# Optimization experiments

Hardware: AMD Instinct MI355X
Metric: run time of the kernel (lower is better)

## Reference

```python
import jax, jax.numpy as jnp
import numpy as np
from jax import lax

C = 16
FIRE_RATE = 0.5
STEP_SIZE = 1.0


def _fixed_kernel():
    _i = np.array([0, 1, 0], dtype=np.float32)
    I = np.outer(_i, _i)
    dx = (np.outer([1, 2, 1], [-1, 0, 1]) / 8.0).astype(np.float32)
    dy = dx.T
    lap = np.array([[0.25, 0.5, 0.25], [0.5, -3, 0.5], [0.25, 0.5, 0.25]], dtype=np.float32)
    av = np.ones((3, 3), dtype=np.float32) / 9.0
    k = np.stack([I, dx, dy, lap, av], -1)            # [3,3,5]
    k = np.tile(k, (1, 1, C))                          # [3,3,5*C], channel-major blocks of 5
    return jnp.asarray(k[:, :, None, :])               # HWIO [3,3,1,5*C]

KERNEL = _fixed_kernel()


def setup_inputs() -> dict:
    key = jax.random.key(0)
    ks = jax.random.split(key, 5)
    B, S = 4, 512
    x = jax.random.normal(ks[0], (B, S, S, C), jnp.float32)
    noise = jax.random.normal(ks[1], (B, S, S, 1), jnp.float32)
    W1 = jax.random.normal(ks[2], (5 * C, 4 * C), jnp.float32) * (1.0 / np.sqrt(5 * C))
    b1 = jnp.zeros((4 * C,), jnp.float32)
    W2 = jax.random.normal(ks[3], (4 * C, 2 * C), jnp.float32) * (1.0 / np.sqrt(4 * C))
    b2 = jnp.zeros((2 * C,), jnp.float32)
    W3 = jax.random.normal(ks[4], (2 * C, C), jnp.float32) * (1.0 / np.sqrt(2 * C))
    b3 = jnp.zeros((C,), jnp.float32)
    return {"x": x, "noise": noise, "W1": W1, "b1": b1, "W2": W2, "b2": b2, "W3": W3, "b3": b3}


def _swish(z):
    return z * jax.nn.sigmoid(z)


def reference(x, noise, W1, b1, W2, b2, W3, b3):
    # perceive: depthwise 3x3 conv with 5 fixed kernels per channel -> [B,H,W,5*C]
    y = lax.conv_general_dilated(
        x, KERNEL, window_strides=(1, 1), padding="SAME",
        dimension_numbers=("NHWC", "HWIO", "NHWC"), feature_group_count=C)
    # 3-layer 1x1 conv MLP
    h = _swish(jnp.einsum("bhwc,cd->bhwd", y, W1) + b1)
    h = _swish(jnp.einsum("bhwc,cd->bhwd", h, W2) + b2)
    dx = (jnp.einsum("bhwc,cd->bhwd", h, W3) + b3) * STEP_SIZE
    # stochastic update mask: normal noise <= fire_rate
    update_mask = (noise <= FIRE_RATE).astype(jnp.float32)  # [B,H,W,1]
    return x + dx * update_mask
```

## Files before the change

kernel.cpp:

```cpp
#include <hip/hip_runtime.h>

typedef __bf16 bf16x8 __attribute__((ext_vector_type(8)));
typedef float f32x16 __attribute__((ext_vector_type(16)));
typedef short short8 __attribute__((ext_vector_type(8)));

#define S 512
#define CH 16

#define ELT(v, c) ((c)==0 ? (v).x : (c)==1 ? (v).y : (c)==2 ? (v).z : (v).w)

__device__ __forceinline__ float swishf(float z) {
    return z * __builtin_amdgcn_rcpf(1.0f + __expf(-z));
}

__global__ void prep_weights(const float* __restrict__ W1, const float* __restrict__ b1,
                             const float* __restrict__ W2, const float* __restrict__ b2,
                             const float* __restrict__ W3, const float* __restrict__ b3,
                             short* __restrict__ wsf, float* __restrict__ wsb)
{
    int idx = blockIdx.x * 256 + threadIdx.x;
    if (idx < 12288) {
        int fi = idx >> 9, rem = idx & 511;
        int lane = rem >> 3, j = rem & 7;
        int col = lane & 31, hi = lane >> 5;
        int jp = (j & 3) + 8 * (j >> 2);
        float v;
        if (fi < 18) {
            int n = fi / 9, s = fi - n * 9;
            int dr = s / 3, dc = s - dr * 3;
            int c = hi * 8 + j;
            const float wgt0 = (dr == 1) ? 2.f : 1.f;
            const float wgt1 = (dc == 1) ? 2.f : 1.f;
            const float dlt0 = (float)(dr - 1);
            const float dlt1 = (float)(dc - 1);
            const float lapm[9] = {0.25f, 0.5f, 0.25f, 0.5f, -3.f, 0.5f, 0.25f, 0.5f, 0.25f};
            float kI  = (s == 4) ? 1.f : 0.f;
            float kdx = wgt0 * dlt1 * 0.125f;
            float kdy = dlt0 * wgt1 * 0.125f;
            float klp = lapm[s];
            float kav = 1.f / 9.f;
            const float* wr = W1 + (c * 5) * 64 + n * 32 + col;
            v = kI * wr[0] + kdx * wr[64] + kdy * wr[128] + klp * wr[192] + kav * wr[256];
        } else if (fi < 22) {
            int t = fi - 18;
            int rowW = (t >> 1) * 32 + 4 * hi + (t & 1) * 16 + jp;
            v = W2[rowW * 32 + col];
        } else {
            int t = fi - 22;
            int rowW = 4 * hi + t * 16 + jp;
            int ch = (col & 3) | (((col >> 3) & 1) << 2) | (((col >> 2) & 1) << 3);
            v = (col < 16) ? W3[rowW * 16 + ch] : 0.0f;
        }
        __bf16 b = (__bf16)v;
        wsf[idx] = __builtin_bit_cast(short, b);
    }
    if (blockIdx.x == 0) {
        int t = threadIdx.x;
        if (t < 64) wsb[t] = b1[t];
        else if (t < 96) wsb[t] = b2[t - 64];
        else if (t < 112) wsb[t] = b3[t - 96];
    }
}

__device__ __forceinline__ void loadrow(const float* __restrict__ xb, int gr, int px0,
                                        int col, int hi, bool edgeStrip, float4 L[3][2])
{
    const bool rv = (unsigned)gr < (unsigned)S;
    const int grc = rv ? gr : (gr < 0 ? 0 : S - 1);
    if (!edgeStrip) {
        const float* rp = xb + ((size_t)grc * S + (px0 + col - 1)) * CH + hi * 8;
#pragma unroll
        for (int dc = 0; dc < 3; ++dc) {
            L[dc][0] = *reinterpret_cast<const float4*>(rp + dc * CH);
            L[dc][1] = *reinterpret_cast<const float4*>(rp + dc * CH + 4);
        }
    } else {
#pragma unroll
        for (int dc = 0; dc < 3; ++dc) {
            int c = px0 + col - 1 + dc;
            bool ok = (unsigned)c < (unsigned)S;
            int cl = min(max(c, 0), S - 1);
            const float* p = xb + ((size_t)grc * S + cl) * CH + hi * 8;
            float4 v0 = *reinterpret_cast<const float4*>(p);
            float4 v1 = *reinterpret_cast<const float4*>(p + 4);
            if (!ok) { v0 = make_float4(0.f, 0.f, 0.f, 0.f); v1 = v0; }
            L[dc][0] = v0; L[dc][1] = v1;
        }
    }
    if (!rv) {
#pragma unroll
        for (int dc = 0; dc < 3; ++dc) {
            L[dc][0] = make_float4(0.f, 0.f, 0.f, 0.f);
            L[dc][1] = L[dc][0];
        }
    }
}

__device__ __forceinline__ short8 cvt2(float4 a, float4 b) {
    short8 f;
    f[0] = __builtin_bit_cast(short, (__bf16)a.x);
    f[1] = __builtin_bit_cast(short, (__bf16)a.y);
    f[2] = __builtin_bit_cast(short, (__bf16)a.z);
    f[3] = __builtin_bit_cast(short, (__bf16)a.w);
    f[4] = __builtin_bit_cast(short, (__bf16)b.x);
    f[5] = __builtin_bit_cast(short, (__bf16)b.y);
    f[6] = __builtin_bit_cast(short, (__bf16)b.z);
    f[7] = __builtin_bit_cast(short, (__bf16)b.w);
    return f;
}

#define NR 8

__global__ __launch_bounds__(256, 3) void nca_fused(
    const float* __restrict__ x, const float* __restrict__ noise,
    const short* __restrict__ wsf, const float* __restrict__ wsb,
    float* __restrict__ out)
{
    __shared__ short wlds[12288];
    {
        const int4* src = reinterpret_cast<const int4*>(wsf);
        int4* dst = reinterpret_cast<int4*>(wlds);
        for (int i = threadIdx.x; i < 1536; i += 256) dst[i] = src[i];
    }
    __syncthreads();

    const int tid = threadIdx.x, bid = blockIdx.x;
    const int wv = tid >> 6, lane = tid & 63;
    const int col = lane & 31, hi = lane >> 5;
    const int st = bid & 15;
    const int rgp = (bid >> 4) & 15;
    const int bb = bid >> 8;
    const int px0 = st * 32;
    const int r0 = (rgp * 4 + wv) * NR;
    const bool edgeStrip = (px0 == 0) || (px0 == 480);
    const float* xb = x + (size_t)bb * S * S * CH;
    const short8* wf = reinterpret_cast<const short8*>(wlds);

    float4 bA = *reinterpret_cast<const float4*>(wsb + 96 + 8 * hi);
    float4 bB = *reinterpret_cast<const float4*>(wsb + 96 + 8 * hi + 4);

    short8 fr[3][3];
    {
        float4 P[3][2];
        loadrow(xb, r0 - 1, px0, col, hi, edgeStrip, P);
#pragma unroll
        for (int dc = 0; dc < 3; ++dc) fr[0][dc] = cvt2(P[dc][0], P[dc][1]);
        loadrow(xb, r0, px0, col, hi, edgeStrip, P);
#pragma unroll
        for (int dc = 0; dc < 3; ++dc) fr[1][dc] = cvt2(P[dc][0], P[dc][1]);
        loadrow(xb, r0 + 1, px0, col, hi, edgeStrip, P);
#pragma unroll
        for (int dc = 0; dc < 3; ++dc) fr[2][dc] = cvt2(P[dc][0], P[dc][1]);
    }

#pragma unroll
    for (int i = 0; i < NR; ++i) {
        const int r = r0 + i;

        float4 NL[3][2];
        loadrow(xb, r + 2, px0, col, hi, edgeStrip, NL);

        const float* cp = xb + ((size_t)r * S + px0 + col) * CH + 8 * hi;
        float4 c0 = *reinterpret_cast<const float4*>(cp);
        float4 c1 = *reinterpret_cast<const float4*>(cp + 4);
        float nz = noise[((size_t)(bb * S + r)) * S + px0 + col];

        f32x16 acc1[2] = {{}, {}};
#pragma unroll
        for (int dr = 0; dr < 3; ++dr)
#pragma unroll
            for (int dc = 0; dc < 3; ++dc) {
                const int s = dr * 3 + dc;
                bf16x8 bfrag = __builtin_bit_cast(bf16x8, fr[(i + dr) % 3][dc]);
                bf16x8 a0 = __builtin_bit_cast(bf16x8, wf[s * 64 + lane]);
                bf16x8 a1 = __builtin_bit_cast(bf16x8, wf[(9 + s) * 64 + lane]);
                acc1[0] = __builtin_amdgcn_mfma_f32_32x32x16_bf16(a0, bfrag, acc1[0], 0, 0, 0);
                acc1[1] = __builtin_amdgcn_mfma_f32_32x32x16_bf16(a1, bfrag, acc1[1], 0, 0, 0);
            }

        short8 b2f[4];
#pragma unroll
        for (int t = 0; t < 4; ++t) {
            int n = t >> 1;
            float4 bq0 = *reinterpret_cast<const float4*>(wsb + n * 32 + 4 * hi + 16 * (t & 1));
            float4 bq1 = *reinterpret_cast<const float4*>(wsb + n * 32 + 4 * hi + 16 * (t & 1) + 8);
#pragma unroll
            for (int j = 0; j < 8; ++j) {
                float bias = (j < 4) ? ELT(bq0, j & 3) : ELT(bq1, j & 3);
                float h = swishf(acc1[n][(t & 1) * 8 + j] + bias);
                b2f[t][j] = __builtin_bit_cast(short, (__bf16)h);
            }
        }

        f32x16 acc2 = {};
#pragma unroll
        for (int t = 0; t < 4; ++t) {
            bf16x8 a = __builtin_bit_cast(bf16x8, wf[(18 + t) * 64 + lane]);
            acc2 = __builtin_amdgcn_mfma_f32_32x32x16_bf16(a, __builtin_bit_cast(bf16x8, b2f[t]), acc2, 0, 0, 0);
        }

        short8 b3f[2];
#pragma unroll
        for (int t = 0; t < 2; ++t) {
            float4 cq0 = *reinterpret_cast<const float4*>(wsb + 64 + 4 * hi + 16 * t);
            float4 cq1 = *reinterpret_cast<const float4*>(wsb + 64 + 4 * hi + 16 * t + 8);
#pragma unroll
            for (int j = 0; j < 8; ++j) {
                float bias = (j < 4) ? ELT(cq0, j & 3) : ELT(cq1, j & 3);
                float h = swishf(acc2[t * 8 + j] + bias);
                b3f[t][j] = __builtin_bit_cast(short, (__bf16)h);
            }
        }

        f32x16 acc3 = {};
#pragma unroll
        for (int t = 0; t < 2; ++t) {
            bf16x8 a = __builtin_bit_cast(bf16x8, wf[(22 + t) * 64 + lane]);
            acc3 = __builtin_amdgcn_mfma_f32_32x32x16_bf16(a, __builtin_bit_cast(bf16x8, b3f[t]), acc3, 0, 0, 0);
        }

        {
            size_t pix = ((size_t)(bb * S + r)) * S + px0 + col;
            float msk = (nz <= 0.5f) ? 1.f : 0.f;
            float4 o0, o1;
            o0.x = c0.x + (acc3[0] + bA.x) * msk;
            o0.y = c0.y + (acc3[1] + bA.y) * msk;
            o0.z = c0.z + (acc3[2] + bA.z) * msk;
            o0.w = c0.w + (acc3[3] + bA.w) * msk;
            o1.x = c1.x + (acc3[4] + bB.x) * msk;
            o1.y = c1.y + (acc3[5] + bB.y) * msk;
            o1.z = c1.z + (acc3[6] + bB.z) * msk;
            o1.w = c1.w + (acc3[7] + bB.w) * msk;
            float* op = out + pix * CH + 8 * hi;
            *reinterpret_cast<float4*>(op) = o0;
            *reinterpret_cast<float4*>(op + 4) = o1;
        }

#pragma unroll
        for (int dc = 0; dc < 3; ++dc)
            fr[i % 3][dc] = cvt2(NL[dc][0], NL[dc][1]);
    }
}

extern "C" void kernel_launch(void* const* d_in, const int* in_sizes, int n_in,
                              void* d_out, int out_size, void* d_ws, size_t ws_size,
                              hipStream_t stream)
{
    const float* x     = (const float*)d_in[0];
    const float* noise = (const float*)d_in[1];
    const float* W1    = (const float*)d_in[2];
    const float* b1    = (const float*)d_in[3];
    const float* W2    = (const float*)d_in[4];
    const float* b2    = (const float*)d_in[5];
    const float* W3    = (const float*)d_in[6];
    const float* b3    = (const float*)d_in[7];
    short* wsf = (short*)d_ws;
    float* wsb = (float*)((char*)d_ws + 24576);
    float* out = (float*)d_out;

    hipLaunchKernelGGL(prep_weights, dim3(48), dim3(256), 0, stream,
                       W1, b1, W2, b2, W3, b3, wsf, wsb);
    hipLaunchKernelGGL(nca_fused, dim3(4 * 16 * 16), dim3(256), 0, stream,
                       x, noise, wsf, wsb, out);
}
```

Before: 208.0 us.

## Halve rows per wave, double grid, XCD-aware block mapping, nontemporal stores

Cuts rows per wave from 8 to 4 and doubles the grid to 2048 blocks, raising the occupancy hint to 4 blocks per CU. Block indices are remapped so the 8 blocks dispatched round-robin across XCDs get adjacent row groups, aiming for better L2 reuse of halo rows. It also skips the dead prefetch of the last row and switches output writes to nontemporal stores to reduce cache pollution. The trade-off is a higher halo reload ratio (6 loaded rows per 4 computed instead of 10 per 8) and tighter register limits.

```diff
diff --git a/kernel.cpp b/kernel.cpp
--- a/kernel.cpp
+++ b/kernel.cpp
@@ -1,6 +1,7 @@
 #include <hip/hip_runtime.h>
 
 typedef __bf16 bf16x8 __attribute__((ext_vector_type(8)));
+typedef float f32x4 __attribute__((ext_vector_type(4)));
 typedef float f32x16 __attribute__((ext_vector_type(16)));
 typedef short short8 __attribute__((ext_vector_type(8)));
 
@@ -109,9 +110,9 @@
     return f;
 }
 
-#define NR 8
-
-__global__ __launch_bounds__(256, 3) void nca_fused(
+#define NR 4
+
+__global__ __launch_bounds__(256, 4) void nca_fused(
     const float* __restrict__ x, const float* __restrict__ noise,
     const short* __restrict__ wsf, const float* __restrict__ wsb,
     float* __restrict__ out)
@@ -127,11 +128,15 @@
     const int tid = threadIdx.x, bid = blockIdx.x;
     const int wv = tid >> 6, lane = tid & 63;
     const int col = lane & 31, hi = lane >> 5;
-    const int st = bid & 15;
-    const int rgp = (bid >> 4) & 15;
-    const int bb = bid >> 8;
+
+    const int xcd = bid & 7;
+    const int k = bid >> 3;
+    const int rg = xcd * 4 + (k & 3);
+    const int sb = k >> 2;
+    const int st = sb & 15;
+    const int bb = sb >> 4;
     const int px0 = st * 32;
-    const int r0 = (rgp * 4 + wv) * NR;
+    const int r0 = rg * 16 + wv * NR;
     const bool edgeStrip = (px0 == 0) || (px0 == 480);
     const float* xb = x + (size_t)bb * S * S * CH;
     const short8* wf = reinterpret_cast<const short8*>(wlds);
@@ -158,7 +163,7 @@
         const int r = r0 + i;
 
         float4 NL[3][2];
-        loadrow(xb, r + 2, px0, col, hi, edgeStrip, NL);
+        if (i + 1 < NR) loadrow(xb, r + 2, px0, col, hi, edgeStrip, NL);
 
         const float* cp = xb + ((size_t)r * S + px0 + col) * CH + 8 * hi;
         float4 c0 = *reinterpret_cast<const float4*>(cp);
@@ -222,23 +227,25 @@
         {
             size_t pix = ((size_t)(bb * S + r)) * S + px0 + col;
             float msk = (nz <= 0.5f) ? 1.f : 0.f;
-            float4 o0, o1;
-            o0.x = c0.x + (acc3[0] + bA.x) * msk;
-            o0.y = c0.y + (acc3[1] + bA.y) * msk;
-            o0.z = c0.z + (acc3[2] + bA.z) * msk;
-            o0.w = c0.w + (acc3[3] + bA.w) * msk;
-            o1.x = c1.x + (acc3[4] + bB.x) * msk;
-            o1.y = c1.y + (acc3[5] + bB.y) * msk;
-            o1.z = c1.z + (acc3[6] + bB.z) * msk;
-            o1.w = c1.w + (acc3[7] + bB.w) * msk;
+            f32x4 o0, o1;
+            o0[0] = c0.x + (acc3[0] + bA.x) * msk;
+            o0[1] = c0.y + (acc3[1] + bA.y) * msk;
+            o0[2] = c0.z + (acc3[2] + bA.z) * msk;
+            o0[3] = c0.w + (acc3[3] + bA.w) * msk;
+            o1[0] = c1.x + (acc3[4] + bB.x) * msk;
+            o1[1] = c1.y + (acc3[5] + bB.y) * msk;
+            o1[2] = c1.z + (acc3[6] + bB.z) * msk;
+            o1[3] = c1.w + (acc3[7] + bB.w) * msk;
             float* op = out + pix * CH + 8 * hi;
-            *reinterpret_cast<float4*>(op) = o0;
-            *reinterpret_cast<float4*>(op + 4) = o1;
-        }
-
-#pragma unroll
-        for (int dc = 0; dc < 3; ++dc)
-            fr[i % 3][dc] = cvt2(NL[dc][0], NL[dc][1]);
+            __builtin_nontemporal_store(o0, reinterpret_cast<f32x4*>(op));
+            __builtin_nontemporal_store(o1, reinterpret_cast<f32x4*>(op + 4));
+        }
+
+        if (i + 1 < NR) {
+#pragma unroll
+            for (int dc = 0; dc < 3; ++dc)
+                fr[i % 3][dc] = cvt2(NL[dc][0], NL[dc][1]);
+        }
     }
 }
 
@@ -260,6 +267,6 @@
 
     hipLaunchKernelGGL(prep_weights, dim3(48), dim3(256), 0, stream,
                        W1, b1, W2, b2, W3, b3, wsf, wsb);
-    hipLaunchKernelGGL(nca_fused, dim3(4 * 16 * 16), dim3(256), 0, stream,
+    hipLaunchKernelGGL(nca_fused, dim3(2048), dim3(256), 0, stream,
                        x, noise, wsf, wsb, out);
 }
```

Result: no change. 206.0 us (-0.9%).
